# Kernel optimization log

Hardware: AMD Instinct MI355X
Metric: run time of the kernel (lower is better)

Reference implementation:

```python
import jax, jax.numpy as jnp
import numpy as np

N, M, D = 8192, 8192, 128

def setup_inputs() -> dict:
    key = jax.random.key(0)
    kq, kk, kv = jax.random.split(key, 3)
    Q = jax.random.normal(kq, (N, D), dtype=jnp.float32)
    K = jax.random.normal(kk, (M, D), dtype=jnp.float32)
    V = jax.random.normal(kv, (M, D), dtype=jnp.float32)
    return {"Q": Q, "K": K, "V": V}

def reference(Q, K, V):
    # scores: [N, M], unscaled QK^T
    scores = Q @ K.T
    # NOTE: original uses torch.softmax(scores, dim=0, dtype=float) -> softmax over the
    # QUERY axis (axis 0), normalizing each key-column across queries.
    attn = jax.nn.softmax(scores.astype(jnp.float32), axis=0)
    return attn @ V  # [N, D]
```

## Files before the change

### kernel.cpp

```cpp
#include <hip/hip_runtime.h>
#include <hip/hip_bf16.h>
#include <math.h>

constexpr int N = 8192, M = 8192, D = 128;
constexpr int NE = N * D;
constexpr float SHIFT = 60.0f;
constexpr float LOG2E = 1.4426950408889634f;
constexpr float S2 = 86.56170245333781f;
constexpr int SN_A = 16;
constexpr int PC_KS = 16;
constexpr int MK = M / 32;

typedef unsigned short u16;
typedef unsigned int u32;
using short8 = __attribute__((ext_vector_type(8))) short;
using f32x4  = __attribute__((ext_vector_type(4))) float;

#define MFMA16(a, b, c) __builtin_amdgcn_mfma_f32_16x16x32_bf16((a), (b), (c), 0, 0, 0)

#if __has_builtin(__builtin_amdgcn_exp2f)
#define EXP2(x) __builtin_amdgcn_exp2f(x)
#else
#define EXP2(x) __expf((x) * 0.6931471805599453f)
#endif

constexpr int PR = 40;
constexpr int KP = 136;
constexpr int WP = 72;
constexpr int PP = 72;

__device__ __forceinline__ u16 f2bf_rn(float x) {
  unsigned int u = __float_as_uint(x);
  return (u16)((u + 0x7fffu + ((u >> 16) & 1u)) >> 16);
}
__device__ __forceinline__ float bf2f(u16 h) { return __uint_as_float((unsigned)h << 16); }

__device__ __forceinline__ size_t qk_frag(int rowblk, int kblk, int lane) {
  return (((size_t)rowblk * 4 + kblk) * 64 + lane) * 8;
}
__device__ __forceinline__ size_t pw_frag(int blk16, int mkblk, int lane) {
  return (((size_t)blk16 * MK + mkblk) * 64 + lane) * 8;
}

__global__ __launch_bounds__(256) void convert_frag(const float4* __restrict__ Qs,
                                                    const float4* __restrict__ Ks,
                                                    u16* __restrict__ Qhi, u16* __restrict__ Qlo,
                                                    u16* __restrict__ Khi, u16* __restrict__ Klo) {
  int idx = blockIdx.x * 256 + threadIdx.x;
  int n = idx >> 4, g = idx & 15;
  const bool isK = blockIdx.y != 0;
  const float4* src = isK ? Ks : Qs;
  u16* hi = isK ? Khi : Qhi;
  u16* lo = isK ? Klo : Qlo;
  const float sc = isK ? 1.0f : LOG2E;
  float4 f0 = src[n * 32 + g * 2], f1 = src[n * 32 + g * 2 + 1];
  float v[8] = {f0.x, f0.y, f0.z, f0.w, f1.x, f1.y, f1.z, f1.w};
  short8 hs, ls;
#pragma unroll
  for (int j = 0; j < 8; ++j) {
    float x = v[j] * sc;
    u16 h = f2bf_rn(x);
    hs[j] = (short)h;
    ls[j] = (short)f2bf_rn(x - bf2f(h));
  }
  size_t off;
  if (isK) {
    int c = n & 1, r = (n & 31) >> 1;
    off = qk_frag((n >> 5) * 2 + c, g >> 2, r + ((g & 3) << 4));
  } else {
    off = qk_frag(n >> 4, g >> 2, (n & 15) + ((g & 3) << 4));
  }
  *(short8*)(hi + off) = hs;
  *(short8*)(lo + off) = ls;
}

__global__ __launch_bounds__(256, 4) void pass_a_frag(const u16* __restrict__ Qh,
                                                      const u16* __restrict__ Ql,
                                                      const u16* __restrict__ Kh,
                                                      const u16* __restrict__ Kl,
                                                      float* __restrict__ colsum,
                                                      u16* __restrict__ Pf) {
  __shared__ u16 PW[4][32 * PR];
  const int tid = threadIdx.x;
  const int w = tid >> 6, lane = tid & 63;
  const int r = lane & 15, q = lane >> 4;
  const int cbase = blockIdx.x * 128 + 32 * w;
  const int mymk = blockIdx.x * 4 + w;
  const int n0 = blockIdx.y * (N / SN_A);
  u16* pw = PW[w];
  u32* pwD = (u32*)pw;

  short8 kh[4][2], kl[4][2];
#pragma unroll
  for (int kk = 0; kk < 4; ++kk)
#pragma unroll
    for (int c = 0; c < 2; ++c) {
      size_t off = qk_frag((cbase >> 4) + c, kk, lane);
      kh[kk][c] = *(const short8*)(Kh + off);
      kl[kk][c] = *(const short8*)(Kl + off);
    }

  float csum[2] = {0.f, 0.f};

  for (int s = 0; s < (N / SN_A) / 32; ++s) {
    const int nb = n0 + s * 32;

    f32x4 acc[2][2];
#pragma unroll
    for (int t = 0; t < 2; ++t)
#pragma unroll
      for (int c = 0; c < 2; ++c) acc[t][c] = (f32x4){-S2, -S2, -S2, -S2};

#pragma unroll
    for (int kk = 0; kk < 4; ++kk) {
      short8 ah[2], al[2];
#pragma unroll
      for (int t = 0; t < 2; ++t) {
        size_t off = qk_frag((nb >> 4) + t, kk, lane);
        ah[t] = *(const short8*)(Qh + off);
        al[t] = *(const short8*)(Ql + off);
      }
#pragma unroll
      for (int t = 0; t < 2; ++t)
#pragma unroll
        for (int c = 0; c < 2; ++c) {
          acc[t][c] = MFMA16(ah[t], kh[kk][c], acc[t][c]);
          acc[t][c] = MFMA16(al[t], kh[kk][c], acc[t][c]);
          acc[t][c] = MFMA16(ah[t], kl[kk][c], acc[t][c]);
        }
    }

#pragma unroll
    for (int t = 0; t < 2; ++t)
#pragma unroll
      for (int rg = 0; rg < 4; ++rg) {
        float e0 = EXP2(acc[t][0][rg]);
        float e1 = EXP2(acc[t][1][rg]);
        csum[0] += e0;
        csum[1] += e1;
        u32 pk = (u32)f2bf_rn(e0) | ((u32)f2bf_rn(e1) << 16);
        pwD[(16 * t + 4 * q + rg) * (PR / 2) + r] = pk;
      }
#pragma unroll
    for (int t = 0; t < 2; ++t) {
      short8 v = *(const short8*)(pw + (16 * t + r) * PR + q * 8);
      *(short8*)(Pf + pw_frag((nb >> 4) + t, mymk, lane)) = v;
    }
  }

  csum[0] += __shfl_xor(csum[0], 16);
  csum[0] += __shfl_xor(csum[0], 32);
  csum[1] += __shfl_xor(csum[1], 16);
  csum[1] += __shfl_xor(csum[1], 32);
  if (lane < 16) {
    atomicAdd(&colsum[cbase + 2 * lane], csum[0]);
    atomicAdd(&colsum[cbase + 2 * lane + 1], csum[1]);
  }
}

__global__ __launch_bounds__(256) void scale_transpose_frag(const float* __restrict__ V,
                                                            const float* __restrict__ colsum,
                                                            u16* __restrict__ Wf) {
  __shared__ float Vs[64][132];
  __shared__ float rls[64];
  const int tid = threadIdx.x;
  const int m0 = blockIdx.x * 64;
#pragma unroll
  for (int it = 0; it < 8; ++it) {
    int idx = tid + it * 256;
    int rr = idx >> 5, g = idx & 31;
    float4 v = *(const float4*)(V + (size_t)(m0 + rr) * D + g * 4);
    Vs[rr][g * 4 + 0] = v.x; Vs[rr][g * 4 + 1] = v.y;
    Vs[rr][g * 4 + 2] = v.z; Vs[rr][g * 4 + 3] = v.w;
  }
  if (tid < 64) rls[tid] = 1.0f / colsum[m0 + tid];
  __syncthreads();
#pragma unroll
  for (int it = 0; it < 4; ++it) {
    int idx = tid + it * 256;
    int dd = idx >> 3, g = idx & 7;
    short8 o;
#pragma unroll
    for (int j = 0; j < 8; ++j) {
      int mm = g * 8 + j;
      o[j] = (short)f2bf_rn(Vs[mm][dd] * rls[mm]);
    }
    *(short8*)(Wf + pw_frag(dd >> 4, (m0 >> 5) + (g >> 2), (dd & 15) + ((g & 3) << 4))) = o;
  }
}

template <bool ATOMIC>
__global__ __launch_bounds__(256, 4) void pass_c_kern(const u16* __restrict__ Pf,
                                                      const u16* __restrict__ Wf,
                                                      float* __restrict__ dst) {
  const int tid = threadIdx.x;
  const int w = tid >> 6, lane = tid & 63;
  const int r = lane & 15, q = lane >> 4;
  const int nblk0 = blockIdx.x * 8 + w * 2;
  const int mk0 = blockIdx.y * (MK / PC_KS);
  constexpr int CNT = MK / PC_KS;

  f32x4 acc[2][8];
#pragma unroll
  for (int i = 0; i < 2; ++i)
#pragma unroll
    for (int dt = 0; dt < 8; ++dt) acc[i][dt] = (f32x4){0.f, 0.f, 0.f, 0.f};

  short8 c0 = *(const short8*)(Pf + pw_frag(nblk0 + 0, mk0, lane));
  short8 c1 = *(const short8*)(Pf + pw_frag(nblk0 + 1, mk0, lane));
  short8 x0 = *(const short8*)(Pf + pw_frag(nblk0 + 0, mk0 + 1, lane));
  short8 x1 = *(const short8*)(Pf + pw_frag(nblk0 + 1, mk0 + 1, lane));

  for (int mk = 0; mk < CNT; ++mk) {
    const int mkg = mk0 + mk;
    const int mk2 = mk + 2 < CNT ? mkg + 2 : mk0;
    short8 p0 = *(const short8*)(Pf + pw_frag(nblk0 + 0, mk2, lane));
    short8 p1 = *(const short8*)(Pf + pw_frag(nblk0 + 1, mk2, lane));
#pragma unroll
    for (int dt = 0; dt < 8; ++dt) {
      short8 b = *(const short8*)(Wf + pw_frag(dt, mkg, lane));
      acc[0][dt] = MFMA16(c0, b, acc[0][dt]);
      acc[1][dt] = MFMA16(c1, b, acc[1][dt]);
    }
    c0 = x0; c1 = x1; x0 = p0; x1 = p1;
  }

  if (ATOMIC) {
#pragma unroll
    for (int i = 0; i < 2; ++i)
#pragma unroll
      for (int dt = 0; dt < 8; ++dt)
#pragma unroll
        for (int rg = 0; rg < 4; ++rg)
          atomicAdd(&dst[(size_t)((nblk0 + i) * 16 + q * 4 + rg) * D + dt * 16 + r],
                    acc[i][dt][rg]);
  } else {
    float* part = dst + (size_t)blockIdx.y * NE;
#pragma unroll
    for (int i = 0; i < 2; ++i)
#pragma unroll
      for (int dt = 0; dt < 8; ++dt)
#pragma unroll
        for (int rg = 0; rg < 4; ++rg)
          part[(size_t)((nblk0 + i) * 16 + q * 4 + rg) * D + dt * 16 + r] = acc[i][dt][rg];
  }
}

__global__ __launch_bounds__(256) void reduce_out(const float4* __restrict__ part,
                                                  float4* __restrict__ out) {
  int i = blockIdx.x * 256 + threadIdx.x;
  float4 s = part[i];
#pragma unroll
  for (int k = 1; k < PC_KS; ++k) {
    float4 p = part[(size_t)k * (NE / 4) + i];
    s.x += p.x; s.y += p.y; s.z += p.z; s.w += p.w;
  }
  out[i] = s;
}

__global__ __launch_bounds__(256) void convert_hilo2(const float4* __restrict__ Qs,
                                                     const float4* __restrict__ Ks,
                                                     ushort4* __restrict__ Qhi, ushort4* __restrict__ Qlo,
                                                     ushort4* __restrict__ Khi, ushort4* __restrict__ Klo) {
  int i = blockIdx.x * 256 + threadIdx.x;
  const float4* src = blockIdx.y ? Ks : Qs;
  ushort4* hi = blockIdx.y ? Khi : Qhi;
  ushort4* lo = blockIdx.y ? Klo : Qlo;
  float4 f = src[i];
  float v[4] = {f.x, f.y, f.z, f.w};
  u16 hs[4], ls[4];
#pragma unroll
  for (int j = 0; j < 4; ++j) {
    hs[j] = f2bf_rn(v[j]);
    ls[j] = f2bf_rn(v[j] - bf2f(hs[j]));
  }
  hi[i] = make_ushort4(hs[0], hs[1], hs[2], hs[3]);
  lo[i] = make_ushort4(ls[0], ls[1], ls[2], ls[3]);
}

__global__ __launch_bounds__(256, 4) void pass_a_fb(const u16* __restrict__ Qh,
                                                    const u16* __restrict__ Ql,
                                                    const u16* __restrict__ Kh,
                                                    const u16* __restrict__ Kl,
                                                    float* __restrict__ colsum) {
  const int tid = threadIdx.x;
  const int w = tid >> 6, lane = tid & 63;
  const int r = lane & 15, q = lane >> 4;
  const int cbase = blockIdx.x * 128 + 32 * w;
  const int n0 = blockIdx.y * (N / 16);

  short8 kh[4][2], kl[4][2];
#pragma unroll
  for (int kk = 0; kk < 4; ++kk)
#pragma unroll
    for (int c = 0; c < 2; ++c) {
      kh[kk][c] = *(const short8*)(Kh + (size_t)(cbase + 16 * c + r) * D + kk * 32 + q * 8);
      kl[kk][c] = *(const short8*)(Kl + (size_t)(cbase + 16 * c + r) * D + kk * 32 + q * 8);
    }

  float csum[2] = {0.f, 0.f};
  for (int s = 0; s < 16; ++s) {
    const int nb = n0 + s * 32;
    f32x4 acc[2][2];
#pragma unroll
    for (int t = 0; t < 2; ++t)
#pragma unroll
      for (int c = 0; c < 2; ++c) acc[t][c] = (f32x4){0.f, 0.f, 0.f, 0.f};
#pragma unroll
    for (int kk = 0; kk < 4; ++kk) {
      short8 ah[2], al[2];
#pragma unroll
      for (int t = 0; t < 2; ++t) {
        ah[t] = *(const short8*)(Qh + (size_t)(nb + t * 16 + r) * D + kk * 32 + q * 8);
        al[t] = *(const short8*)(Ql + (size_t)(nb + t * 16 + r) * D + kk * 32 + q * 8);
      }
#pragma unroll
      for (int t = 0; t < 2; ++t)
#pragma unroll
        for (int c = 0; c < 2; ++c) {
          acc[t][c] = MFMA16(ah[t], kh[kk][c], acc[t][c]);
          acc[t][c] = MFMA16(al[t], kh[kk][c], acc[t][c]);
          acc[t][c] = MFMA16(ah[t], kl[kk][c], acc[t][c]);
        }
    }
#pragma unroll
    for (int t = 0; t < 2; ++t)
#pragma unroll
      for (int c = 0; c < 2; ++c)
#pragma unroll
        for (int rg = 0; rg < 4; ++rg) csum[c] += __expf(acc[t][c][rg] - SHIFT);
  }
  csum[0] += __shfl_xor(csum[0], 16);
  csum[0] += __shfl_xor(csum[0], 32);
  csum[1] += __shfl_xor(csum[1], 16);
  csum[1] += __shfl_xor(csum[1], 32);
  if (lane < 16) {
    atomicAdd(&colsum[cbase + r], csum[0]);
    atomicAdd(&colsum[cbase + 16 + r], csum[1]);
  }
}

__global__ __launch_bounds__(256) void scale_transpose_fb(const float* __restrict__ V,
                                                          const float* __restrict__ colsum,
                                                          u16* __restrict__ Wt) {
  __shared__ float Vs[64][132];
  __shared__ float rls[64];
  const int tid = threadIdx.x;
  const int m0 = blockIdx.x * 64;
#pragma unroll
  for (int it = 0; it < 8; ++it) {
    int idx = tid + it * 256;
    int rr = idx >> 5, g = idx & 31;
    float4 v = *(const float4*)(V + (size_t)(m0 + rr) * D + g * 4);
    Vs[rr][g * 4 + 0] = v.x; Vs[rr][g * 4 + 1] = v.y;
    Vs[rr][g * 4 + 2] = v.z; Vs[rr][g * 4 + 3] = v.w;
  }
  if (tid < 64) rls[tid] = 1.0f / colsum[m0 + tid];
  __syncthreads();
#pragma unroll
  for (int it = 0; it < 4; ++it) {
    int idx = tid + it * 256;
    int dd = idx >> 3, g = idx & 7;
    short8 o;
#pragma unroll
    for (int j = 0; j < 8; ++j) {
      int mm = g * 8 + j;
      o[j] = (short)f2bf_rn(Vs[mm][dd] * rls[mm]);
    }
    *(short8*)(Wt + (size_t)dd * M + m0 + g * 8) = o;
  }
}

__global__ __launch_bounds__(256, 2) void pass_c_fb(const u16* __restrict__ Qh,
                                                    const u16* __restrict__ Ql,
                                                    const u16* __restrict__ Kh,
                                                    const u16* __restrict__ Kl,
                                                    const u16* __restrict__ Wt,
                                                    float* __restrict__ out) {
  __shared__ u16 KsH[64 * KP];
  __shared__ u16 KsL[64 * KP];
  __shared__ u16 Ws[128 * WP];
  __shared__ u16 Ps[4][16 * PP];
  const int tid = threadIdx.x;
  const int w = tid >> 6, lane = tid & 63;
  const int r = lane & 15, q = lane >> 4;
  const size_t nrow = (size_t)blockIdx.x * 64 + w * 16 + r;
  const int mbase = blockIdx.y * (M / 4);

  short8 qh[4], ql[4];
#pragma unroll
  for (int kk = 0; kk < 4; ++kk) {
    qh[kk] = *(const short8*)(Qh + nrow * D + kk * 32 + q * 8);
    ql[kk] = *(const short8*)(Ql + nrow * D + kk * 32 + q * 8);
  }

  f32x4 oacc[8];
#pragma unroll
  for (int dt = 0; dt < 8; ++dt) oacc[dt] = (f32x4){0.f, 0.f, 0.f, 0.f};

  for (int mt = 0; mt < (M / 4) / 64; ++mt) {
    const int m0 = mbase + mt * 64;
    __syncthreads();
#pragma unroll
    for (int it = 0; it < 4; ++it) {
      int idx = tid + it * 256;
      int rr = idx >> 4, g = idx & 15;
      *(short8*)(KsH + rr * KP + g * 8) = *(const short8*)(Kh + (size_t)(m0 + rr) * D + g * 8);
      *(short8*)(KsL + rr * KP + g * 8) = *(const short8*)(Kl + (size_t)(m0 + rr) * D + g * 8);
    }
#pragma unroll
    for (int it = 0; it < 4; ++it) {
      int idx = tid + it * 256;
      int dd = idx >> 3, g = idx & 7;
      *(short8*)(Ws + dd * WP + g * 8) = *(const short8*)(Wt + (size_t)dd * M + m0 + g * 8);
    }
    __syncthreads();

    f32x4 sacc[4];
#pragma unroll
    for (int t = 0; t < 4; ++t) sacc[t] = (f32x4){0.f, 0.f, 0.f, 0.f};
#pragma unroll
    for (int kk = 0; kk < 4; ++kk) {
      short8 bh[4], bl[4];
#pragma unroll
      for (int t = 0; t < 4; ++t) {
        bh[t] = *(const short8*)(KsH + (t * 16 + r) * KP + kk * 32 + q * 8);
        bl[t] = *(const short8*)(KsL + (t * 16 + r) * KP + kk * 32 + q * 8);
      }
#pragma unroll
      for (int t = 0; t < 4; ++t) {
        sacc[t] = MFMA16(qh[kk], bh[t], sacc[t]);
        sacc[t] = MFMA16(qh[kk], bl[t], sacc[t]);
        sacc[t] = MFMA16(ql[kk], bh[t], sacc[t]);
      }
    }
#pragma unroll
    for (int t = 0; t < 4; ++t)
#pragma unroll
      for (int rg = 0; rg < 4; ++rg)
        Ps[w][(q * 4 + rg) * PP + t * 16 + r] = f2bf_rn(__expf(sacc[t][rg] - SHIFT));
#pragma unroll
    for (int kk = 0; kk < 2; ++kk) {
      short8 pa = *(const short8*)(Ps[w] + r * PP + kk * 32 + q * 8);
#pragma unroll
      for (int dt = 0; dt < 8; ++dt) {
        short8 wb = *(const short8*)(Ws + (dt * 16 + r) * WP + kk * 32 + q * 8);
        oacc[dt] = MFMA16(pa, wb, oacc[dt]);
      }
    }
  }
#pragma unroll
  for (int dt = 0; dt < 8; ++dt)
#pragma unroll
    for (int rg = 0; rg < 4; ++rg)
      atomicAdd(&out[((size_t)blockIdx.x * 64 + w * 16 + q * 4 + rg) * D + dt * 16 + r],
                oacc[dt][rg]);
}

extern "C" void kernel_launch(void* const* d_in, const int* in_sizes, int n_in,
                              void* d_out, int out_size, void* d_ws, size_t ws_size,
                              hipStream_t stream) {
  const float* Q = (const float*)d_in[0];
  const float* K = (const float*)d_in[1];
  const float* V = (const float*)d_in[2];
  float* out = (float*)d_out;

  u16* Qh = (u16*)d_ws;
  u16* Ql = Qh + NE;
  u16* Kh = Ql + NE;
  u16* Kl = Kh + NE;
  u16* Wb = Kl + NE;
  float* colsum = (float*)(Wb + NE);
  u16* Pf = (u16*)(colsum + M);
  float* Opart = (float*)(Pf + (size_t)N * M);
  const size_t need_mat = (size_t)5 * NE * 2 + M * 4 + (size_t)N * M * 2;
  const size_t need_part = need_mat + (size_t)PC_KS * NE * 4;
  const bool mat = ws_size >= need_mat;
  const bool part = ws_size >= need_part;

  hipMemsetAsync(colsum, 0, M * sizeof(float), stream);
  if (!part) hipMemsetAsync(d_out, 0, (size_t)N * D * sizeof(float), stream);

  if (mat) {
    convert_frag<<<dim3(N * 16 / 256, 2), 256, 0, stream>>>(
        (const float4*)Q, (const float4*)K, Qh, Ql, Kh, Kl);
    pass_a_frag<<<dim3(M / 128, SN_A), 256, 0, stream>>>(Qh, Ql, Kh, Kl, colsum, Pf);
    scale_transpose_frag<<<M / 64, 256, 0, stream>>>(V, colsum, Wb);
    if (part) {
      pass_c_kern<false><<<dim3(N / 128, PC_KS), 256, 0, stream>>>(Pf, Wb, Opart);
      reduce_out<<<NE / 4 / 256, 256, 0, stream>>>((const float4*)Opart, (float4*)out);
    } else {
      pass_c_kern<true><<<dim3(N / 128, PC_KS), 256, 0, stream>>>(Pf, Wb, out);
    }
  } else {
    convert_hilo2<<<dim3(NE / 4 / 256, 2), 256, 0, stream>>>(
        (const float4*)Q, (const float4*)K, (ushort4*)Qh, (ushort4*)Ql, (ushort4*)Kh, (ushort4*)Kl);
    pass_a_fb<<<dim3(M / 128, 16), 256, 0, stream>>>(Qh, Ql, Kh, Kl, colsum);
    scale_transpose_fb<<<M / 64, 256, 0, stream>>>(V, colsum, Wb);
    pass_c_fb<<<dim3(N / 64, 4), 256, 0, stream>>>(Qh, Ql, Kh, Kl, Wb, out);
  }
}
```

Baseline: 176.2 us.

## Stage convert through LDS, fold colsum zeroing, double-buffer pass A, halve split-K

The conversion kernel now reads Q/K rows coalesced into LDS, splits them into bf16 hi/lo there, and writes the MFMA fragment layout from LDS. It also zeroes colsum, which removes the separate memset launch. Pass A double-buffers its per-wave LDS staging tile so consecutive iterations need not wait on each other, and pass C's split-K factor drops from 16 to 8, shrinking the partial buffer and the reduction. Zeroing colsum inside block 0 relies on that kernel finishing before pass A reads colsum, and the doubled LDS in pass A may reduce occupancy.

```diff
diff --git a/kernel.cpp b/kernel.cpp
--- a/kernel.cpp
+++ b/kernel.cpp
@@ -8,7 +8,7 @@
 constexpr float LOG2E = 1.4426950408889634f;
 constexpr float S2 = 86.56170245333781f;
 constexpr int SN_A = 16;
-constexpr int PC_KS = 16;
+constexpr int PC_KS = 8;
 constexpr int MK = M / 32;
 
 typedef unsigned short u16;
@@ -25,6 +25,7 @@
 #endif
 
 constexpr int PR = 40;
+constexpr int CP = 136;
 constexpr int KP = 136;
 constexpr int WP = 72;
 constexpr int PP = 72;
@@ -42,36 +43,64 @@
   return (((size_t)blk16 * MK + mkblk) * 64 + lane) * 8;
 }
 
-__global__ __launch_bounds__(256) void convert_frag(const float4* __restrict__ Qs,
-                                                    const float4* __restrict__ Ks,
-                                                    u16* __restrict__ Qhi, u16* __restrict__ Qlo,
-                                                    u16* __restrict__ Khi, u16* __restrict__ Klo) {
-  int idx = blockIdx.x * 256 + threadIdx.x;
-  int n = idx >> 4, g = idx & 15;
+__global__ __launch_bounds__(256) void convert_frag2(const float4* __restrict__ Qs,
+                                                     const float4* __restrict__ Ks,
+                                                     u16* __restrict__ Qhi, u16* __restrict__ Qlo,
+                                                     u16* __restrict__ Khi, u16* __restrict__ Klo,
+                                                     float* __restrict__ colsum) {
+  __shared__ u16 LH[64 * CP];
+  __shared__ u16 LL[64 * CP];
+  const int tid = threadIdx.x;
   const bool isK = blockIdx.y != 0;
   const float4* src = isK ? Ks : Qs;
   u16* hi = isK ? Khi : Qhi;
   u16* lo = isK ? Klo : Qlo;
   const float sc = isK ? 1.0f : LOG2E;
-  float4 f0 = src[n * 32 + g * 2], f1 = src[n * 32 + g * 2 + 1];
-  float v[8] = {f0.x, f0.y, f0.z, f0.w, f1.x, f1.y, f1.z, f1.w};
-  short8 hs, ls;
-#pragma unroll
-  for (int j = 0; j < 8; ++j) {
-    float x = v[j] * sc;
-    u16 h = f2bf_rn(x);
-    hs[j] = (short)h;
-    ls[j] = (short)f2bf_rn(x - bf2f(h));
-  }
-  size_t off;
-  if (isK) {
-    int c = n & 1, r = (n & 31) >> 1;
-    off = qk_frag((n >> 5) * 2 + c, g >> 2, r + ((g & 3) << 4));
-  } else {
-    off = qk_frag(n >> 4, g >> 2, (n & 15) + ((g & 3) << 4));
-  }
-  *(short8*)(hi + off) = hs;
-  *(short8*)(lo + off) = ls;
+  const int row0 = blockIdx.x * 64;
+
+  if (blockIdx.x == 0 && !isK) {
+#pragma unroll
+    for (int k = 0; k < M / 256; ++k) colsum[tid + k * 256] = 0.f;
+  }
+
+#pragma unroll
+  for (int it = 0; it < 8; ++it) {
+    int idx = tid + it * 256;
+    int rr = idx >> 5, g = idx & 31;
+    float4 f = src[(size_t)(row0 + rr) * 32 + g];
+    float v[4] = {f.x, f.y, f.z, f.w};
+    u16 h[4], l4[4];
+#pragma unroll
+    for (int j = 0; j < 4; ++j) {
+      float x = v[j] * sc;
+      h[j] = f2bf_rn(x);
+      l4[j] = f2bf_rn(x - bf2f(h[j]));
+    }
+    u32* ph = (u32*)(LH + rr * CP + g * 4);
+    u32* pl = (u32*)(LL + rr * CP + g * 4);
+    ph[0] = (u32)h[0] | ((u32)h[1] << 16);
+    ph[1] = (u32)h[2] | ((u32)h[3] << 16);
+    pl[0] = (u32)l4[0] | ((u32)l4[1] << 16);
+    pl[1] = (u32)l4[2] | ((u32)l4[3] << 16);
+  }
+  __syncthreads();
+
+#pragma unroll
+  for (int it = 0; it < 4; ++it) {
+    int idx = tid + it * 256;
+    int tau = idx >> 6, l = idx & 63;
+    int rowblk = tau >> 2, kblk = tau & 3;
+    int d = kblk * 32 + (l >> 4) * 8;
+    int nl;
+    if (isK) {
+      nl = ((rowblk >> 1) << 5) + ((l & 15) << 1) + (rowblk & 1);
+    } else {
+      nl = rowblk * 16 + (l & 15);
+    }
+    size_t off = qk_frag((row0 >> 4) + rowblk, kblk, l);
+    *(short8*)(hi + off) = *(const short8*)(LH + nl * CP + d);
+    *(short8*)(lo + off) = *(const short8*)(LL + nl * CP + d);
+  }
 }
 
 __global__ __launch_bounds__(256, 4) void pass_a_frag(const u16* __restrict__ Qh,
@@ -80,15 +109,13 @@
                                                       const u16* __restrict__ Kl,
                                                       float* __restrict__ colsum,
                                                       u16* __restrict__ Pf) {
-  __shared__ u16 PW[4][32 * PR];
+  __shared__ u16 PW[4][2][32 * PR];
   const int tid = threadIdx.x;
   const int w = tid >> 6, lane = tid & 63;
   const int r = lane & 15, q = lane >> 4;
   const int cbase = blockIdx.x * 128 + 32 * w;
   const int mymk = blockIdx.x * 4 + w;
   const int n0 = blockIdx.y * (N / SN_A);
-  u16* pw = PW[w];
-  u32* pwD = (u32*)pw;
 
   short8 kh[4][2], kl[4][2];
 #pragma unroll
@@ -102,8 +129,11 @@
 
   float csum[2] = {0.f, 0.f};
 
+#pragma unroll 2
   for (int s = 0; s < (N / SN_A) / 32; ++s) {
     const int nb = n0 + s * 32;
+    u16* pw = PW[w][s & 1];
+    u32* pwD = (u32*)pw;
 
     f32x4 acc[2][2];
 #pragma unroll
@@ -478,21 +508,21 @@
   const bool mat = ws_size >= need_mat;
   const bool part = ws_size >= need_part;
 
-  hipMemsetAsync(colsum, 0, M * sizeof(float), stream);
-  if (!part) hipMemsetAsync(d_out, 0, (size_t)N * D * sizeof(float), stream);
-
   if (mat) {
-    convert_frag<<<dim3(N * 16 / 256, 2), 256, 0, stream>>>(
-        (const float4*)Q, (const float4*)K, Qh, Ql, Kh, Kl);
+    convert_frag2<<<dim3(N / 64, 2), 256, 0, stream>>>(
+        (const float4*)Q, (const float4*)K, Qh, Ql, Kh, Kl, colsum);
     pass_a_frag<<<dim3(M / 128, SN_A), 256, 0, stream>>>(Qh, Ql, Kh, Kl, colsum, Pf);
     scale_transpose_frag<<<M / 64, 256, 0, stream>>>(V, colsum, Wb);
     if (part) {
       pass_c_kern<false><<<dim3(N / 128, PC_KS), 256, 0, stream>>>(Pf, Wb, Opart);
       reduce_out<<<NE / 4 / 256, 256, 0, stream>>>((const float4*)Opart, (float4*)out);
     } else {
+      hipMemsetAsync(d_out, 0, (size_t)N * D * sizeof(float), stream);
       pass_c_kern<true><<<dim3(N / 128, PC_KS), 256, 0, stream>>>(Pf, Wb, out);
     }
   } else {
+    hipMemsetAsync(colsum, 0, M * sizeof(float), stream);
+    hipMemsetAsync(d_out, 0, (size_t)N * D * sizeof(float), stream);
     convert_hilo2<<<dim3(NE / 4 / 256, 2), 256, 0, stream>>>(
         (const float4*)Q, (const float4*)K, (ushort4*)Qh, (ushort4*)Ql, (ushort4*)Kh, (ushort4*)Kl);
     pass_a_fb<<<dim3(M / 128, 16), 256, 0, stream>>>(Qh, Ql, Kh, Kl, colsum);
```

After: 173.0 us. No clear change (-1.8%).
